# Kernel tuning notes

Hardware: AMD Instinct MI355X
Metric: run time of the kernel (lower is better)

## Reference

```python
import jax, jax.numpy as jnp
import numpy as np

EPS_RMS = 1e-6
EPS_Q = 1e-5
EPS_NORM = 1e-10


def _rmsnorm(x):
    return x * jax.lax.rsqrt(jnp.mean(x * x, axis=-1, keepdims=True) + EPS_RMS)


def _activation_quant(x):
    # per-token 8-bit absmax quantization (BitNet b1.58)
    scale = 127.0 / jnp.maximum(jnp.max(jnp.abs(x), axis=-1, keepdims=True), EPS_Q)
    return jnp.clip(jnp.round(x * scale), -128.0, 127.0) / scale


def _weight_quant(w):
    # per-tensor ternary quantization with mean-abs scale
    scale = 1.0 / jnp.maximum(jnp.mean(jnp.abs(w)), EPS_Q)
    return jnp.clip(jnp.round(w * scale), -1.0, 1.0) / scale


def _bitlinear(x, w, b):
    xn = _rmsnorm(x)
    xq = xn + jax.lax.stop_gradient(_activation_quant(xn) - xn)  # STE
    wq = w + jax.lax.stop_gradient(_weight_quant(w) - w)         # STE
    return jnp.einsum('bsf,of->bso', xq, wq) + b


def setup_inputs() -> dict:
    key = jax.random.key(0)
    ks = jax.random.split(key, 4)
    B, S, F = 32, 1024, 512
    evidence_features = jax.random.normal(ks[0], (B, S, F), dtype=jnp.float32)
    prior_belief = jax.random.uniform(ks[1], (B, S, F), dtype=jnp.float32)
    W1 = jax.random.normal(ks[2], (F, 2 * F), dtype=jnp.float32) * (1.0 / np.sqrt(2 * F))
    b1 = jnp.zeros((F,), dtype=jnp.float32)
    W2 = jax.random.normal(ks[3], (F, F), dtype=jnp.float32) * (1.0 / np.sqrt(F))
    b2 = jnp.zeros((F,), dtype=jnp.float32)
    return {"evidence_features": evidence_features, "prior_belief": prior_belief,
            "W1": W1, "b1": b1, "W2": W2, "b2": b2}


def reference(evidence_features, prior_belief, W1, b1, W2, b2):
    # belief_update MLP on concat(prior, evidence)
    update_input = jnp.concatenate([prior_belief, evidence_features], axis=-1)  # [B,S,2F]
    h = jax.nn.relu(_bitlinear(update_input, W1, b1))                           # [B,S,F]
    likelihood_factors = jax.nn.sigmoid(_bitlinear(h, W2, b2))                  # [B,S,F]
    posterior_unnorm = prior_belief * likelihood_factors
    normalizer = jnp.maximum(jnp.sum(posterior_unnorm, axis=1, keepdims=True), EPS_NORM)
    return posterior_unnorm / normalizer
```

## Files before the change

### kernel.cpp

```cpp
#include <hip/hip_runtime.h>
#include <math.h>

typedef __attribute__((ext_vector_type(4))) int i32x4;
typedef __attribute__((ext_vector_type(4))) float f32x4;

#define GLOAD_LDS16(g, l)                                          \
  __builtin_amdgcn_global_load_lds(                                \
      (const __attribute__((address_space(1))) void*)(g),          \
      (__attribute__((address_space(3))) void*)(l), 16, 0, 0)

__global__ void kWabs(const float* __restrict__ w, int n, double* __restrict__ part) {
  int t = blockIdx.x * 256 + threadIdx.x;
  double s = 0.0;
  for (int i = t; i < n; i += 65536) s += (double)fabsf(w[i]);
#pragma unroll
  for (int m = 32; m >= 1; m >>= 1) s += __shfl_xor(s, m);
  __shared__ double sd[4];
  int lane = threadIdx.x & 63, wid = threadIdx.x >> 6;
  if (lane == 0) sd[wid] = s;
  __syncthreads();
  if (threadIdx.x == 0) part[blockIdx.x] = (sd[0] + sd[1]) + (sd[2] + sd[3]);
}

__global__ void kWfin(const double* __restrict__ p1, const double* __restrict__ p2,
                      float* __restrict__ wsv) {
  const double* p = (blockIdx.x == 0) ? p1 : p2;
  const double n = (blockIdx.x == 0) ? 524288.0 : 262144.0;
  double s = p[threadIdx.x];
#pragma unroll
  for (int m = 32; m >= 1; m >>= 1) s += __shfl_xor(s, m);
  __shared__ double sd[4];
  int lane = threadIdx.x & 63, wid = threadIdx.x >> 6;
  if (lane == 0) sd[wid] = s;
  __syncthreads();
  if (threadIdx.x == 0) {
    double tot = (sd[0] + sd[1]) + (sd[2] + sd[3]);
    wsv[blockIdx.x] = fmaxf((float)(tot / n), 1e-5f);
  }
}

__global__ void kWq(const float* __restrict__ w, int n, const float* __restrict__ wsv,
                    char* __restrict__ wq) {
  int i = blockIdx.x * 256 + threadIdx.x;
  if (i >= n) return;
  float scale = 1.0f / wsv[0];
  float q = fminf(fmaxf(rintf(w[i] * scale), -1.0f), 1.0f);
  wq[i] = (char)(int)q;
}

__global__ void kQ1(const float* __restrict__ prior, const float* __restrict__ evid,
                    char* __restrict__ Xq, float* __restrict__ rAct) {
  const int row = blockIdx.x;
  const int t = threadIdx.x;
  const f32x4* src = (t < 128) ? (const f32x4*)(prior + (size_t)row * 512)
                               : (const f32x4*)(evid + (size_t)row * 512);
  f32x4 x = src[t & 127];
  float ss = 0.f, mx = 0.f;
#pragma unroll
  for (int i = 0; i < 4; ++i) { ss += x[i] * x[i]; mx = fmaxf(mx, fabsf(x[i])); }
#pragma unroll
  for (int m = 32; m >= 1; m >>= 1) { ss += __shfl_xor(ss, m); mx = fmaxf(mx, __shfl_xor(mx, m)); }
  __shared__ float sss[4], smx[4];
  const int lane = t & 63, wid = t >> 6;
  if (lane == 0) { sss[wid] = ss; smx[wid] = mx; }
  __syncthreads();
  ss = (sss[0] + sss[1]) + (sss[2] + sss[3]);
  mx = fmaxf(fmaxf(smx[0], smx[1]), fmaxf(smx[2], smx[3]));
  const float inv = 1.0f / sqrtf(ss * (1.0f / 1024.0f) + 1e-6f);
  const float amax = fmaxf(mx * inv, 1e-5f);
  const float s = 127.0f / amax;
  int pack = 0;
#pragma unroll
  for (int i = 0; i < 4; ++i) {
    float xn = x[i] * inv;
    int qi = (int)fminf(fmaxf(rintf(xn * s), -128.0f), 127.0f);
    pack |= (qi & 255) << (8 * i);
  }
  *(int*)(Xq + (size_t)row * 1024 + t * 4) = pack;
  if (t == 0) rAct[row] = amax / 127.0f;
}

template <int KDIM, bool L1>
__global__ __launch_bounds__(512, 4) void kGemm(
    const char* __restrict__ Xq, const char* __restrict__ Wq,
    const float* __restrict__ biasG, const float* __restrict__ rAct,
    const float* __restrict__ wS,
    char* __restrict__ XqOut, float* __restrict__ rActOut,
    const float* __restrict__ prior, float* __restrict__ outUn,
    float* __restrict__ partG) {
  __shared__ __align__(16) union {
    struct { char A[4096]; char B[32768]; } st;
    struct { float sq[64][8]; float mx[64][8]; } ep;
  } u;
  __shared__ float rowR[64];
  __shared__ float biasS[512];
  __shared__ float normPart[512];

  const int tid = threadIdx.x;
  const int lane = tid & 63;
  const int wn = tid >> 6;
  const int lr = lane & 15;
  const int kg = lane >> 4;
  const size_t row0 = (size_t)blockIdx.x * 64;

  if (tid < 64) rowR[tid] = rAct[row0 + tid];
  biasS[tid] = biasG[tid];

  i32x4 acc[4][4];
#pragma unroll
  for (int a = 0; a < 4; ++a)
#pragma unroll
    for (int b = 0; b < 4; ++b) acc[a][b] = (i32x4){0, 0, 0, 0};

  const int lrow = lane >> 2;
  const int lkb = (lane & 3) * 16;

  for (int kt = 0; kt < KDIM / 64; ++kt) {
    const int k0 = kt * 64;
    if (wn < 4) {
      const char* g = Xq + (row0 + wn * 16 + lrow) * (size_t)KDIM + k0 + lkb;
      GLOAD_LDS16(g, &u.st.A[wn * 1024]);
    }
#pragma unroll
    for (int r = 0; r < 4; ++r) {
      const int c = wn * 4 + r;
      const char* g = Wq + (c * 16 + lrow) * (size_t)KDIM + k0 + lkb;
      GLOAD_LDS16(g, &u.st.B[c * 1024]);
    }
    __syncthreads();
    i32x4 af[4];
#pragma unroll
    for (int fm = 0; fm < 4; ++fm)
      af[fm] = *(const i32x4*)&u.st.A[(fm * 16 + lr) * 64 + kg * 16];
#pragma unroll
    for (int fn = 0; fn < 4; ++fn) {
      i32x4 bf = *(const i32x4*)&u.st.B[(wn * 64 + fn * 16 + lr) * 64 + kg * 16];
#pragma unroll
      for (int fm = 0; fm < 4; ++fm)
        acc[fm][fn] = __builtin_amdgcn_mfma_i32_16x16x64_i8(af[fm], bf, acc[fm][fn], 0, 0, 0);
    }
    __syncthreads();
  }

  const float wsv_ = wS[0];

  if constexpr (L1) {
    f32x4 fa[4][4];
#pragma unroll
    for (int fm = 0; fm < 4; ++fm) {
      float sc[4];
#pragma unroll
      for (int j = 0; j < 4; ++j) sc[j] = rowR[fm * 16 + kg * 4 + j] * wsv_;
#pragma unroll
      for (int fn = 0; fn < 4; ++fn) {
        const float bb = biasS[wn * 64 + fn * 16 + lr];
#pragma unroll
        for (int j = 0; j < 4; ++j)
          fa[fm][fn][j] = fmaxf((float)acc[fm][fn][j] * sc[j] + bb, 0.0f);
      }
    }
#pragma unroll
    for (int fm = 0; fm < 4; ++fm)
#pragma unroll
      for (int j = 0; j < 4; ++j) {
        float ss = 0.f, mx = 0.f;
#pragma unroll
        for (int fn = 0; fn < 4; ++fn) { float h = fa[fm][fn][j]; ss += h * h; mx = fmaxf(mx, h); }
#pragma unroll
        for (int m = 8; m >= 1; m >>= 1) { ss += __shfl_xor(ss, m); mx = fmaxf(mx, __shfl_xor(mx, m)); }
        if (lr == 0) {
          int rl = fm * 16 + kg * 4 + j;
          u.ep.sq[rl][wn] = ss;
          u.ep.mx[rl][wn] = mx;
        }
      }
    __syncthreads();
#pragma unroll
    for (int fm = 0; fm < 4; ++fm)
#pragma unroll
      for (int j = 0; j < 4; ++j) {
        const int rl = fm * 16 + kg * 4 + j;
        float sst = 0.f, mxt = 0.f;
#pragma unroll
        for (int w = 0; w < 8; ++w) {
          sst += u.ep.sq[rl][w];
          mxt = fmaxf(mxt, u.ep.mx[rl][w]);
        }
        float inv = 1.0f / sqrtf(sst * (1.0f / 512.0f) + 1e-6f);
        float amax = fmaxf(mxt * inv, 1e-5f);
        float s = 127.0f / amax;
        if (lr == 0 && wn == 0) rActOut[row0 + rl] = amax / 127.0f;
#pragma unroll
        for (int fn = 0; fn < 4; ++fn) {
          float xn = fa[fm][fn][j] * inv;
          int qi = (int)fminf(fmaxf(rintf(xn * s), -128.0f), 127.0f);
          XqOut[(row0 + rl) * 512 + wn * 64 + fn * 16 + lr] = (char)qi;
        }
      }
  } else {
    float colsum[4] = {0.f, 0.f, 0.f, 0.f};
#pragma unroll
    for (int fm = 0; fm < 4; ++fm) {
      float sc[4];
#pragma unroll
      for (int j = 0; j < 4; ++j) sc[j] = rowR[fm * 16 + kg * 4 + j] * wsv_;
#pragma unroll
      for (int fn = 0; fn < 4; ++fn) {
        const int col = wn * 64 + fn * 16 + lr;
        const float bb = biasS[col];
#pragma unroll
        for (int j = 0; j < 4; ++j) {
          const size_t rg = row0 + fm * 16 + kg * 4 + j;
          float v = (float)acc[fm][fn][j] * sc[j] + bb;
          float like = 1.0f / (1.0f + expf(-v));
          float un = prior[rg * 512 + col] * like;
          outUn[rg * 512 + col] = un;
          colsum[fn] += un;
        }
      }
    }
#pragma unroll
    for (int fn = 0; fn < 4; ++fn) {
      colsum[fn] += __shfl_xor(colsum[fn], 16);
      colsum[fn] += __shfl_xor(colsum[fn], 32);
    }
    if (lane < 16) {
#pragma unroll
      for (int fn = 0; fn < 4; ++fn) normPart[wn * 64 + fn * 16 + lane] = colsum[fn];
    }
    __syncthreads();
    partG[(size_t)blockIdx.x * 512 + tid] = normPart[tid];
  }
}

__global__ void kNorm1(const float* __restrict__ partG, float* __restrict__ normA) {
  const int b = blockIdx.x, f = threadIdx.x;
  float s = 0.f;
#pragma unroll
  for (int i = 0; i < 16; ++i) s += partG[(size_t)(b * 16 + i) * 512 + f];
  normA[b * 512 + f] = fmaxf(s, 1e-10f);
}

__global__ void kNorm2(float* __restrict__ out, const float* __restrict__ normA) {
  const size_t i4 = (size_t)blockIdx.x * blockDim.x + threadIdx.x;
  f32x4 v = ((const f32x4*)out)[i4];
  const int f4 = (int)(i4 & 127);
  const int b = (int)(i4 >> 17);
  f32x4 n = ((const f32x4*)normA)[b * 128 + f4];
  v[0] /= n[0]; v[1] /= n[1]; v[2] /= n[2]; v[3] /= n[3];
  ((f32x4*)out)[i4] = v;
}

extern "C" void kernel_launch(void* const* d_in, const int* in_sizes, int n_in,
                              void* d_out, int out_size, void* d_ws, size_t ws_size,
                              hipStream_t stream) {
  const float* evid  = (const float*)d_in[0];
  const float* prior = (const float*)d_in[1];
  const float* W1    = (const float*)d_in[2];
  const float* b1    = (const float*)d_in[3];
  const float* W2    = (const float*)d_in[4];
  const float* b2    = (const float*)d_in[5];
  float* out = (float*)d_out;

  char* ws = (char*)d_ws;
  char*   X2q   = ws;
  char*   W1q   = ws + 16777216;
  char*   W2q   = ws + 17301504;
  float*  r1    = (float*)(ws + 17563648);
  float*  r2    = (float*)(ws + 17694720);
  double* p1    = (double*)(ws + 17825792);
  double* p2    = (double*)(ws + 17827840);
  float*  wsv   = (float*)(ws + 17829888);
  float*  partG = (float*)(ws + 17830144);
  float*  normA = (float*)(ws + 18878720);

  char* X1q = (char*)d_out;

  kWabs<<<256, 256, 0, stream>>>(W1, 524288, p1);
  kWabs<<<256, 256, 0, stream>>>(W2, 262144, p2);
  kWfin<<<2, 256, 0, stream>>>(p1, p2, wsv);
  kWq<<<2048, 256, 0, stream>>>(W1, 524288, wsv + 0, W1q);
  kWq<<<1024, 256, 0, stream>>>(W2, 262144, wsv + 1, W2q);
  kQ1<<<32768, 256, 0, stream>>>(prior, evid, X1q, r1);
  kGemm<1024, true><<<512, 512, 0, stream>>>(X1q, W1q, b1, r1, wsv + 0,
                                             X2q, r2, nullptr, nullptr, nullptr);
  kGemm<512, false><<<512, 512, 0, stream>>>(X2q, W2q, b2, r2, wsv + 1,
                                             nullptr, nullptr, prior, out, partG);
  kNorm1<<<32, 512, 0, stream>>>(partG, normA);
  kNorm2<<<16384, 256, 0, stream>>>(out, normA);
}
```

Measured before the change: 149.7 us.

## Double-buffer LDS tiles in int8 GEMM to overlap loads with MFMA

Splits the shared-memory staging area into two buffers. The next K-tile is prefetched via global_load_lds while MFMAs run on the current tile, and the loop drops from two barriers per iteration to one. Global pointers are hoisted out of the loop. This doubles LDS staging use (about 73KB), which may lower occupancy below the launch_bounds target of 4 blocks per CU.

```diff
diff --git a/kernel.cpp b/kernel.cpp
--- a/kernel.cpp
+++ b/kernel.cpp
@@ -88,8 +88,9 @@
     char* __restrict__ XqOut, float* __restrict__ rActOut,
     const float* __restrict__ prior, float* __restrict__ outUn,
     float* __restrict__ partG) {
+  struct Stage { char A[4096]; char B[32768]; };
   __shared__ __align__(16) union {
-    struct { char A[4096]; char B[32768]; } st;
+    Stage st[2];
     struct { float sq[64][8]; float mx[64][8]; } ep;
   } u;
   __shared__ float rowR[64];
@@ -115,32 +116,42 @@
   const int lrow = lane >> 2;
   const int lkb = (lane & 3) * 16;
 
-  for (int kt = 0; kt < KDIM / 64; ++kt) {
-    const int k0 = kt * 64;
-    if (wn < 4) {
-      const char* g = Xq + (row0 + wn * 16 + lrow) * (size_t)KDIM + k0 + lkb;
-      GLOAD_LDS16(g, &u.st.A[wn * 1024]);
-    }
-#pragma unroll
-    for (int r = 0; r < 4; ++r) {
-      const int c = wn * 4 + r;
-      const char* g = Wq + (c * 16 + lrow) * (size_t)KDIM + k0 + lkb;
-      GLOAD_LDS16(g, &u.st.B[c * 1024]);
-    }
-    __syncthreads();
+  const char* gA = Xq + (row0 + (wn & 3) * 16 + lrow) * (size_t)KDIM + lkb;
+  const char* gB[4];
+#pragma unroll
+  for (int r = 0; r < 4; ++r)
+    gB[r] = Wq + ((wn * 4 + r) * 16 + lrow) * (size_t)KDIM + lkb;
+
+#define STAGE(b, k0)                                                   \
+  do {                                                                 \
+    if (wn < 4) GLOAD_LDS16(gA + (k0), &u.st[b].A[(wn & 3) * 1024]);   \
+    _Pragma("unroll")                                                  \
+    for (int r = 0; r < 4; ++r)                                        \
+      GLOAD_LDS16(gB[r] + (k0), &u.st[b].B[(wn * 4 + r) * 1024]);      \
+  } while (0)
+
+  constexpr int NT = KDIM / 64;
+  STAGE(0, 0);
+  __syncthreads();
+
+#pragma unroll 2
+  for (int kt = 0; kt < NT; ++kt) {
+    const int cur = kt & 1;
+    if (kt + 1 < NT) STAGE(cur ^ 1, (kt + 1) * 64);
     i32x4 af[4];
 #pragma unroll
     for (int fm = 0; fm < 4; ++fm)
-      af[fm] = *(const i32x4*)&u.st.A[(fm * 16 + lr) * 64 + kg * 16];
+      af[fm] = *(const i32x4*)&u.st[cur].A[(fm * 16 + lr) * 64 + kg * 16];
 #pragma unroll
     for (int fn = 0; fn < 4; ++fn) {
-      i32x4 bf = *(const i32x4*)&u.st.B[(wn * 64 + fn * 16 + lr) * 64 + kg * 16];
+      i32x4 bf = *(const i32x4*)&u.st[cur].B[(wn * 64 + fn * 16 + lr) * 64 + kg * 16];
 #pragma unroll
       for (int fm = 0; fm < 4; ++fm)
         acc[fm][fn] = __builtin_amdgcn_mfma_i32_16x16x64_i8(af[fm], bf, acc[fm][fn], 0, 0, 0);
     }
     __syncthreads();
   }
+#undef STAGE
 
   const float wsv_ = wS[0];
 
```

After: 140.1 us. -6.4%, faster.
